# Kernel tuning notes

Hardware: AMD Instinct MI355X
Metric: run time of the kernel (lower is better)

## Reference

```python
import jax, jax.numpy as jnp
import numpy as np

B, S, HID = 2, 2048, 2048
NH, NKV, HD = 16, 8, 128
GROUPS = NH // NKV
EPS = 1e-6
SCALE = HD ** -0.5
ROPE_THETA = 1000000.0


def _rope_cos_sin(seq_len, head_dim, batch):
    inv_freq = 1.0 / (ROPE_THETA ** (np.arange(0, head_dim, 2, dtype=np.float32) / head_dim))
    t = np.arange(seq_len, dtype=np.float32)
    freqs = np.outer(t, inv_freq)                      # [S, HD/2]
    emb = np.concatenate([freqs, freqs], axis=-1)      # [S, HD]
    cos = np.broadcast_to(np.cos(emb), (batch, seq_len, head_dim))
    sin = np.broadcast_to(np.sin(emb), (batch, seq_len, head_dim))
    return jnp.asarray(cos), jnp.asarray(sin)


def setup_inputs() -> dict:
    key = jax.random.key(0)
    ks = jax.random.split(key, 6)
    hidden_states = jax.random.normal(ks[0], (B, S, HID), dtype=jnp.float32)
    cos, sin = _rope_cos_sin(S, HD, B)
    w_scale = HID ** -0.5
    Wq = jax.random.normal(ks[1], (NH * HD, HID), dtype=jnp.float32) * w_scale
    Wk = jax.random.normal(ks[2], (NKV * HD, HID), dtype=jnp.float32) * w_scale
    Wv = jax.random.normal(ks[3], (NKV * HD, HID), dtype=jnp.float32) * w_scale
    Wo = jax.random.normal(ks[4], (HID, NH * HD), dtype=jnp.float32) * w_scale
    q_norm_w = jnp.ones((HD,), dtype=jnp.float32)
    k_norm_w = jnp.ones((HD,), dtype=jnp.float32)
    return {"hidden_states": hidden_states, "cos": cos, "sin": sin,
            "Wq": Wq, "Wk": Wk, "Wv": Wv, "Wo": Wo,
            "q_norm_w": q_norm_w, "k_norm_w": k_norm_w}


def _rms_norm(x, w):
    # RMSNorm over last dim (head_dim), variance computed in fp32
    var = jnp.mean(x.astype(jnp.float32) ** 2, axis=-1, keepdims=True)
    return w * (x * jax.lax.rsqrt(var + EPS).astype(x.dtype))


def _rotate_half(x):
    x1, x2 = jnp.split(x, 2, axis=-1)
    return jnp.concatenate([-x2, x1], axis=-1)


def _apply_rope(x, cos, sin):
    # x: [B, H, S, D]; cos/sin: [B, S, D] -> unsqueeze head dim
    c = cos[:, None, :, :]
    s = sin[:, None, :, :]
    return x * c + _rotate_half(x) * s


def reference(hidden_states, cos, sin, Wq, Wk, Wv, Wo, q_norm_w, k_norm_w):
    b, s, _ = hidden_states.shape
    # QKV projections (bias=False per config.attention_bias)
    q = (hidden_states @ Wq.T).reshape(b, s, NH, HD)
    k = (hidden_states @ Wk.T).reshape(b, s, NKV, HD)
    v = (hidden_states @ Wv.T).reshape(b, s, NKV, HD)
    # Per-head QK RMSNorm, then [B, H, S, D]
    q = _rms_norm(q, q_norm_w).transpose(0, 2, 1, 3)
    k = _rms_norm(k, k_norm_w).transpose(0, 2, 1, 3)
    v = v.transpose(0, 2, 1, 3)
    # RoPE
    q = _apply_rope(q, cos, sin)
    k = _apply_rope(k, cos, sin)
    # GQA: expand kv heads to match query heads
    k = jnp.repeat(k, GROUPS, axis=1)
    v = jnp.repeat(v, GROUPS, axis=1)
    # SDPA (is_causal=False, mask=None, dropout=0)
    scores = jnp.einsum('bhqd,bhkd->bhqk', q, k) * SCALE
    probs = jax.nn.softmax(scores, axis=-1)
    attn = jnp.einsum('bhqk,bhkd->bhqd', probs, v)
    attn = attn.transpose(0, 2, 1, 3).reshape(b, s, NH * HD)
    return attn @ Wo.T
```

## Files before the change

kernel.cpp:

```cpp
#include <hip/hip_runtime.h>

using short8 = __attribute__((ext_vector_type(8))) short;
using f32x4  = __attribute__((ext_vector_type(4))) float;
using u32x2  = __attribute__((ext_vector_type(2))) unsigned int;
using u32x4  = __attribute__((ext_vector_type(4))) unsigned int;

#define MFMA16(a, b, c) __builtin_amdgcn_mfma_f32_16x16x32_bf16((a), (b), (c), 0, 0, 0)

__device__ inline float bf2f(ushort v) { return __uint_as_float(((unsigned int)v) << 16); }
__device__ inline unsigned int f2bfu(float f) {
  unsigned int u = __float_as_uint(f);
  return (u + 0x7fffu + ((u >> 16) & 1u)) >> 16;
}
__device__ inline unsigned int pk2(float a, float b) { return f2bfu(a) | (f2bfu(b) << 16); }

__device__ inline void gl_lds16(const ushort* g, ushort* l) {
  __builtin_amdgcn_global_load_lds(
      (const __attribute__((address_space(1))) void*)g,
      (__attribute__((address_space(3))) void*)l, 16, 0, 0);
}

__global__ __launch_bounds__(256) void f2b8(const float* __restrict__ src,
                                            ushort* __restrict__ dst, int n) {
  int i = (blockIdx.x * 256 + threadIdx.x) * 8;
  if (i >= n) return;
  f32x4 a = *(const f32x4*)(src + i);
  f32x4 b = *(const f32x4*)(src + i + 4);
  u32x4 o;
  o[0] = pk2(a[0], a[1]); o[1] = pk2(a[2], a[3]);
  o[2] = pk2(b[0], b[1]); o[3] = pk2(b[2], b[3]);
  *(u32x4*)(dst + i) = o;
}

#define GPHASE(CB, P, STG, VMW)                                                     \
  {                                                                                 \
    if (P == 0) {                                                                   \
      _Pragma("unroll") for (int n = 0; n < 4; ++n) {                               \
        bf[n][0] = *(const short8*)&L[(CB)*32768 + bBase + n*1024 + rdoff];         \
        bf[n][1] = *(const short8*)&L[(CB)*32768 + bBase + n*1024 + (rdoff ^ 32)];  \
      }                                                                             \
    }                                                                               \
    short8 af[2][2];                                                                \
    _Pragma("unroll") for (int mi = 0; mi < 2; ++mi) {                              \
      af[mi][0] = *(const short8*)&L[(CB)*32768 + aBase + ((P)*2+mi)*1024 + rdoff];        \
      af[mi][1] = *(const short8*)&L[(CB)*32768 + aBase + ((P)*2+mi)*1024 + (rdoff ^ 32)]; \
    }                                                                               \
    STG;                                                                            \
    __builtin_amdgcn_s_barrier();                                                   \
    asm volatile("s_waitcnt lgkmcnt(0)" ::: "memory");                              \
    __builtin_amdgcn_s_setprio(1);                                                  \
    _Pragma("unroll") for (int mi = 0; mi < 2; ++mi)                                \
      _Pragma("unroll") for (int n = 0; n < 4; ++n) {                               \
        acc[(P)*2+mi][n] = MFMA16(af[mi][0], bf[n][0], acc[(P)*2+mi][n]);           \
        acc[(P)*2+mi][n] = MFMA16(af[mi][1], bf[n][1], acc[(P)*2+mi][n]);           \
      }                                                                             \
    __builtin_amdgcn_s_setprio(0);                                                  \
    VMW;                                                                            \
    __builtin_amdgcn_s_barrier();                                                   \
  }

#define VM4 asm volatile("s_waitcnt vmcnt(4)" ::: "memory")
#define NOPX (void)0

template <int OUTF32>
__global__ __launch_bounds__(512, 2) void gemm256(const ushort* __restrict__ A,
                                                  const ushort* __restrict__ B,
                                                  void* __restrict__ Cv,
                                                  int M, int N, int K) {
  __shared__ ushort L[65536];
  const int t = threadIdx.x;
  const int w = t >> 6, l = t & 63, lr = l & 15, lg = l >> 4;
  const int wr = w >> 2, wc = w & 3;
  const int m0 = blockIdx.x * 256, n0 = blockIdx.y * 256;
  const int NT = K >> 6, NI = NT >> 1;

  f32x4 acc[8][4] = {};

  const int rdoff = lr * 64 + ((lg ^ (lr & 7)) * 8);
  const int aBase = wr * 8192;
  const int bBase = 16384 + (wc >> 1) * 8192 + (wc & 1) * 4096;

  const int ch0 = w * 2, ch1 = w * 2 + 1;
  const int srow0 = ch0 * 8 + (l >> 3), srow1 = ch1 * 8 + (l >> 3);
  const int scol = ((l & 7) ^ (l >> 3)) * 8;

  auto stage_a = [&](int h, int kt, int cb) {
    int ktc = kt < NT ? kt : NT - 1;
    gl_lds16(A + (size_t)(m0 + h * 128 + srow0) * K + ktc * 64 + scol,
             (ushort*)&L[cb * 32768 + h * 8192 + ch0 * 512]);
    gl_lds16(A + (size_t)(m0 + h * 128 + srow1) * K + ktc * 64 + scol,
             (ushort*)&L[cb * 32768 + h * 8192 + ch1 * 512]);
  };
  auto stage_b = [&](int h, int kt, int cb) {
    int ktc = kt < NT ? kt : NT - 1;
    gl_lds16(B + (size_t)(n0 + h * 128 + srow0) * K + ktc * 64 + scol,
             (ushort*)&L[cb * 32768 + 16384 + h * 8192 + ch0 * 512]);
    gl_lds16(B + (size_t)(n0 + h * 128 + srow1) * K + ktc * 64 + scol,
             (ushort*)&L[cb * 32768 + 16384 + h * 8192 + ch1 * 512]);
  };

  stage_a(0, 0, 0); stage_a(1, 0, 0); stage_b(0, 0, 0); stage_b(1, 0, 0);
  stage_b(0, 1, 1); stage_b(1, 1, 1);
  VM4;
  __builtin_amdgcn_s_barrier();

  short8 bf[4][2];
  for (int I = 0; I < NI; ++I) {
    const int t1 = 2 * I + 1, t2 = 2 * I + 2, t3 = 2 * I + 3;
    GPHASE(0, 0, stage_a(0, t1, 1), NOPX)
    GPHASE(0, 1, stage_a(1, t1, 1), NOPX)
    GPHASE(0, 2, stage_b(0, t2, 0), NOPX)
    GPHASE(0, 3, stage_b(1, t2, 0), VM4)
    GPHASE(1, 0, stage_a(0, t2, 0), NOPX)
    GPHASE(1, 1, stage_a(1, t2, 0), NOPX)
    GPHASE(1, 2, stage_b(0, t3, 1), NOPX)
    GPHASE(1, 3, stage_b(1, t3, 1), VM4)
  }

  const int crow0 = m0 + wr * 128 + lg * 4;
  const int ccol = n0 + wc * 64 + lr;
  if (OUTF32) {
    float* C = (float*)Cv;
#pragma unroll
    for (int m = 0; m < 8; ++m)
#pragma unroll
      for (int n = 0; n < 4; ++n)
#pragma unroll
        for (int j = 0; j < 4; ++j)
          C[(size_t)(crow0 + m * 16 + j) * N + ccol + n * 16] = acc[m][n][j];
  } else {
    ushort* C = (ushort*)Cv;
#pragma unroll
    for (int m = 0; m < 8; ++m)
#pragma unroll
      for (int n = 0; n < 4; ++n)
#pragma unroll
        for (int j = 0; j < 4; ++j)
          C[(size_t)(crow0 + m * 16 + j) * N + ccol + n * 16] = (ushort)f2bfu(acc[m][n][j]);
  }
}

__global__ __launch_bounds__(256) void qk_norm_rope(
    const ushort* __restrict__ QKVp, const float* __restrict__ cosb,
    const float* __restrict__ sinb, const float* __restrict__ qw,
    const float* __restrict__ kw, ushort* __restrict__ Qa, ushort* __restrict__ Ka) {
  int r = blockIdx.x * 4 + (threadIdx.x >> 6);
  int i = threadIdx.x & 63;
  int b, s, srccol;
  ushort* dst;
  const float* w;
  float scale;
  if (r < 65536) {
    b = r >> 15; int rem = r & 32767; s = rem >> 4; int h = rem & 15;
    srccol = h * 128;
    dst = Qa + ((size_t)((b * 16 + h) * 2048 + s)) * 128;
    w = qw;
    scale = 0.08838834764831845f * 1.4426950408889634f;
  } else {
    int rk = r - 65536;
    b = rk >> 14; int rem = rk & 16383; s = rem >> 3; int kvh = rem & 7;
    srccol = 2048 + kvh * 128;
    dst = Ka + ((size_t)((b * 8 + kvh) * 2048 + s)) * 128;
    w = kw;
    scale = 1.0f;
  }
  const ushort* src = QKVp + ((size_t)(b * 2048 + s)) * 4096 + srccol;
  float x0 = bf2f(src[i]), x1 = bf2f(src[i + 64]);
  float ss = x0 * x0 + x1 * x1;
#pragma unroll
  for (int m = 1; m < 64; m <<= 1) ss += __shfl_xor(ss, m);
  float inv = rsqrtf(ss * (1.0f / 128.0f) + 1e-6f);
  float xn0 = x0 * inv * w[i], xn1 = x1 * inv * w[i + 64];
  const float* cp = cosb + ((size_t)(b * 2048 + s)) * 128;
  const float* sp = sinb + ((size_t)(b * 2048 + s)) * 128;
  float o0 = (xn0 * cp[i] - xn1 * sp[i]) * scale;
  float o1 = (xn1 * cp[i + 64] + xn0 * sp[i + 64]) * scale;
  dst[i] = (ushort)f2bfu(o0);
  dst[i + 64] = (ushort)f2bfu(o1);
}

__global__ __launch_bounds__(256) void v_transpose(const ushort* __restrict__ QKVp,
                                                   ushort* __restrict__ Vt) {
  __shared__ ushort tile[64][136];
  int blk = blockIdx.x;
  int st = blk & 31, kvh = (blk >> 5) & 7, b = blk >> 8;
  int t = threadIdx.x;
  int s0 = st * 64;
  {
    int r = t >> 2, cseg = (t & 3) * 32;
    const ushort* src = QKVp + ((size_t)(b * 2048 + s0 + r)) * 4096 + 3072 + kvh * 128 + cseg;
#pragma unroll
    for (int i = 0; i < 4; ++i)
      *(uint4*)&tile[r][cseg + i * 8] = *(const uint4*)(src + i * 8);
  }
  __syncthreads();
  {
    int d = t >> 1, sh = (t & 1) * 32;
    ushort* dst = Vt + ((size_t)((b * 8 + kvh) * 128 + d)) * 2048 + s0 + sh;
    ushort buf[32];
#pragma unroll
    for (int k = 0; k < 32; ++k) buf[k] = tile[sh + k][d];
#pragma unroll
    for (int i = 0; i < 4; ++i) *(uint4*)(dst + i * 8) = *(uint4*)&buf[i * 8];
  }
}

__global__ __launch_bounds__(256, 2) void attn_kernel(const ushort* __restrict__ Qa,
                                                      const ushort* __restrict__ Ka,
                                                      const ushort* __restrict__ Vt,
                                                      ushort* __restrict__ Ctx) {
  __shared__ ushort Ks[64 * 128];
  __shared__ ushort Vs[128 * 64];
  __shared__ ushort Ps[8 * 1024];
  const int bh = blockIdx.x, b = bh >> 4, h = bh & 15, kvh = h >> 1;
  const int t = threadIdx.x, w = t >> 6, l = t & 63, lr = l & 15, lg = l >> 4;
  const int q0 = blockIdx.y * 128 + w * 32;
  const ushort* Qh = Qa + ((size_t)(b * 16 + h)) * 2048 * 128;
  const ushort* Kh = Ka + ((size_t)(b * 8 + kvh)) * 2048 * 128;
  const ushort* Vh = Vt + ((size_t)(b * 8 + kvh)) * 128 * 2048;

  short8 bq[2][4];
#pragma unroll
  for (int qt = 0; qt < 2; ++qt)
#pragma unroll
    for (int dc = 0; dc < 4; ++dc)
      bq[qt][dc] = *(const short8*)&Qh[(size_t)(q0 + qt * 16 + lr) * 128 + dc * 32 + lg * 8];

  f32x4 accO[8][2] = {};
  float mrun[2] = {-3.0e38f, -3.0e38f};
  float lrun[2] = {0.f, 0.f};

  for (int kt0 = 0; kt0 < 2048; kt0 += 64) {
    __syncthreads();
#pragma unroll
    for (int i = 0; i < 4; ++i) {
      const int c = w * 4 + i;
      const int krow = c * 4 + lg;
      gl_lds16(Kh + (size_t)(kt0 + krow) * 128 + (((l & 15) ^ (krow & 7)) * 8),
               &Ks[c * 512]);
      const int vrow = c * 8 + (l >> 3);
      gl_lds16(Vh + (size_t)vrow * 2048 + kt0 + (((l & 7) ^ ((l >> 3) & 7)) * 8),
               &Vs[c * 512]);
    }
    asm volatile("s_waitcnt vmcnt(0)" ::: "memory");
    __syncthreads();

    f32x4 accS[4][2] = {};
#pragma unroll
    for (int dc = 0; dc < 4; ++dc) {
      short8 ak[4];
#pragma unroll
      for (int kts = 0; kts < 4; ++kts)
        ak[kts] = *(const short8*)&Ks[(kts * 16 + lr) * 128 + ((dc * 4 + lg) ^ (lr & 7)) * 8];
#pragma unroll
      for (int kts = 0; kts < 4; ++kts)
#pragma unroll
        for (int qt = 0; qt < 2; ++qt)
          accS[kts][qt] = MFMA16(ak[kts], bq[qt][dc], accS[kts][qt]);
    }

#pragma unroll
    for (int qt = 0; qt < 2; ++qt) {
      float m0 = fmaxf(fmaxf(accS[0][qt][0], accS[0][qt][1]), fmaxf(accS[0][qt][2], accS[0][qt][3]));
      float m1 = fmaxf(fmaxf(accS[1][qt][0], accS[1][qt][1]), fmaxf(accS[1][qt][2], accS[1][qt][3]));
      float m2 = fmaxf(fmaxf(accS[2][qt][0], accS[2][qt][1]), fmaxf(accS[2][qt][2], accS[2][qt][3]));
      float m3 = fmaxf(fmaxf(accS[3][qt][0], accS[3][qt][1]), fmaxf(accS[3][qt][2], accS[3][qt][3]));
      float tm = fmaxf(fmaxf(m0, m1), fmaxf(m2, m3));
      tm = fmaxf(tm, __shfl_xor(tm, 16));
      tm = fmaxf(tm, __shfl_xor(tm, 32));
      if (!__all(tm <= mrun[qt] + 11.0f)) {
        float nm = fmaxf(mrun[qt], tm);
        float cf = exp2f(mrun[qt] - nm);
#pragma unroll
        for (int dc = 0; dc < 8; ++dc) {
          accO[dc][qt][0] *= cf; accO[dc][qt][1] *= cf;
          accO[dc][qt][2] *= cf; accO[dc][qt][3] *= cf;
        }
        lrun[qt] *= cf;
        mrun[qt] = nm;
      }
      float ts = 0.f;
#pragma unroll
      for (int kts = 0; kts < 4; ++kts)
#pragma unroll
        for (int j = 0; j < 4; ++j) {
          float p = exp2f(accS[kts][qt][j] - mrun[qt]);
          accS[kts][qt][j] = p;
          ts += p;
        }
      ts += __shfl_xor(ts, 16);
      ts += __shfl_xor(ts, 32);
      lrun[qt] += ts;
#pragma unroll
      for (int kts = 0; kts < 4; ++kts) {
        u32x2 pv;
        pv[0] = pk2(accS[kts][qt][0], accS[kts][qt][1]);
        pv[1] = pk2(accS[kts][qt][2], accS[kts][qt][3]);
        *(u32x2*)&Ps[(w * 2 + qt) * 1024 + lr * 64 +
                     (((kts * 2 + (lg >> 1)) ^ (lr & 7)) * 8 + (lg & 1) * 4)] = pv;
      }
    }
    asm volatile("s_waitcnt lgkmcnt(0)" ::: "memory");

    short8 bp[2][2];
#pragma unroll
    for (int qt = 0; qt < 2; ++qt)
#pragma unroll
      for (int ks = 0; ks < 2; ++ks)
        bp[qt][ks] = *(const short8*)&Ps[(w * 2 + qt) * 1024 + lr * 64 +
                                         ((ks * 4 + lg) ^ (lr & 7)) * 8];
#pragma unroll
    for (int dc = 0; dc < 8; ++dc) {
      short8 av[2];
#pragma unroll
      for (int ks = 0; ks < 2; ++ks)
        av[ks] = *(const short8*)&Vs[(dc * 16 + lr) * 64 + ((ks * 4 + lg) ^ (lr & 7)) * 8];
#pragma unroll
      for (int ks = 0; ks < 2; ++ks)
#pragma unroll
        for (int qt = 0; qt < 2; ++qt)
          accO[dc][qt] = MFMA16(av[ks], bp[qt][ks], accO[dc][qt]);
    }
  }

#pragma unroll
  for (int qt = 0; qt < 2; ++qt) {
    float inv = 1.0f / lrun[qt];
    int srow = q0 + qt * 16 + lr;
#pragma unroll
    for (int dc = 0; dc < 8; ++dc) {
      u32x2 ov;
      ov[0] = pk2(accO[dc][qt][0] * inv, accO[dc][qt][1] * inv);
      ov[1] = pk2(accO[dc][qt][2] * inv, accO[dc][qt][3] * inv);
      *(u32x2*)&Ctx[(size_t)(b * 2048 + srow) * 2048 + h * 128 + dc * 16 + lg * 4] = ov;
    }
  }
}

extern "C" void kernel_launch(void* const* d_in, const int* in_sizes, int n_in,
                              void* d_out, int out_size, void* d_ws, size_t ws_size,
                              hipStream_t stream) {
  const float* hidden = (const float*)d_in[0];
  const float* cosb   = (const float*)d_in[1];
  const float* sinb   = (const float*)d_in[2];
  const float* Wq     = (const float*)d_in[3];
  const float* Wk     = (const float*)d_in[4];
  const float* Wv     = (const float*)d_in[5];
  const float* Wo     = (const float*)d_in[6];
  const float* qw     = (const float*)d_in[7];
  const float* kw     = (const float*)d_in[8];

  char* ws = (char*)d_ws;
  ushort* Xb    = (ushort*)ws; ws += (size_t)4096 * 2048 * 2;
  ushort* Wcomb = (ushort*)ws; ws += (size_t)4096 * 2048 * 2;
  ushort* Wob   = (ushort*)ws; ws += (size_t)2048 * 2048 * 2;
  ushort* QKVp  = (ushort*)ws; ws += (size_t)4096 * 4096 * 2;
  ushort* Qa    = (ushort*)ws; ws += (size_t)2 * 16 * 2048 * 128 * 2;
  ushort* Ka    = (ushort*)ws; ws += (size_t)2 * 8 * 2048 * 128 * 2;
  ushort* Vt    = (ushort*)ws; ws += (size_t)2 * 8 * 2048 * 128 * 2;
  ushort* Ctx   = (ushort*)ws; ws += (size_t)4096 * 2048 * 2;

  f2b8<<<4096, 256, 0, stream>>>(hidden, Xb, 8388608);
  f2b8<<<2048, 256, 0, stream>>>(Wq, Wcomb, 4194304);
  f2b8<<<1024, 256, 0, stream>>>(Wk, Wcomb + 4194304, 2097152);
  f2b8<<<1024, 256, 0, stream>>>(Wv, Wcomb + 6291456, 2097152);
  f2b8<<<2048, 256, 0, stream>>>(Wo, Wob, 4194304);

  gemm256<0><<<dim3(16, 16), 512, 0, stream>>>(Xb, Wcomb, (void*)QKVp, 4096, 4096, 2048);

  qk_norm_rope<<<24576, 256, 0, stream>>>(QKVp, cosb, sinb, qw, kw, Qa, Ka);
  v_transpose<<<512, 256, 0, stream>>>(QKVp, Vt);

  attn_kernel<<<dim3(32, 16), 256, 0, stream>>>(Qa, Ka, Vt, Ctx);

  gemm256<1><<<dim3(16, 8), 512, 0, stream>>>(Ctx, Wob, d_out, 4096, 2048, 2048);
}
```

Baseline: 379.1 us.

## Double-buffer K/V tiles in attention kernel and use native exp2

```diff
diff --git a/kernel.cpp b/kernel.cpp
--- a/kernel.cpp
+++ b/kernel.cpp
@@ -209,8 +209,8 @@
                                                       const ushort* __restrict__ Ka,
                                                       const ushort* __restrict__ Vt,
                                                       ushort* __restrict__ Ctx) {
-  __shared__ ushort Ks[64 * 128];
-  __shared__ ushort Vs[128 * 64];
+  __shared__ ushort Ks[2][64 * 128];
+  __shared__ ushort Vs[2][128 * 64];
   __shared__ ushort Ps[8 * 1024];
   const int bh = blockIdx.x, b = bh >> 4, h = bh & 15, kvh = h >> 1;
   const int t = threadIdx.x, w = t >> 6, l = t & 63, lr = l & 15, lg = l >> 4;
@@ -225,33 +225,33 @@
 #pragma unroll
     for (int dc = 0; dc < 4; ++dc)
       bq[qt][dc] = *(const short8*)&Qh[(size_t)(q0 + qt * 16 + lr) * 128 + dc * 32 + lg * 8];
+  asm volatile("s_waitcnt vmcnt(0)" ::: "memory");
 
   f32x4 accO[8][2] = {};
   float mrun[2] = {-3.0e38f, -3.0e38f};
   float lrun[2] = {0.f, 0.f};
 
-  for (int kt0 = 0; kt0 < 2048; kt0 += 64) {
-    __syncthreads();
+  auto stage = [&](int kt0, ushort* KSB, ushort* VSB) {
 #pragma unroll
     for (int i = 0; i < 4; ++i) {
       const int c = w * 4 + i;
       const int krow = c * 4 + lg;
       gl_lds16(Kh + (size_t)(kt0 + krow) * 128 + (((l & 15) ^ (krow & 7)) * 8),
-               &Ks[c * 512]);
+               KSB + c * 512);
       const int vrow = c * 8 + (l >> 3);
       gl_lds16(Vh + (size_t)vrow * 2048 + kt0 + (((l & 7) ^ ((l >> 3) & 7)) * 8),
-               &Vs[c * 512]);
-    }
-    asm volatile("s_waitcnt vmcnt(0)" ::: "memory");
-    __syncthreads();
-
+               VSB + c * 512);
+    }
+  };
+
+  auto iter = [&](int kt, const ushort* KSB, const ushort* VSB, ushort* KSN, ushort* VSN) {
     f32x4 accS[4][2] = {};
 #pragma unroll
     for (int dc = 0; dc < 4; ++dc) {
       short8 ak[4];
 #pragma unroll
       for (int kts = 0; kts < 4; ++kts)
-        ak[kts] = *(const short8*)&Ks[(kts * 16 + lr) * 128 + ((dc * 4 + lg) ^ (lr & 7)) * 8];
+        ak[kts] = *(const short8*)&KSB[(kts * 16 + lr) * 128 + ((dc * 4 + lg) ^ (lr & 7)) * 8];
 #pragma unroll
       for (int kts = 0; kts < 4; ++kts)
 #pragma unroll
@@ -270,7 +270,7 @@
       tm = fmaxf(tm, __shfl_xor(tm, 32));
       if (!__all(tm <= mrun[qt] + 11.0f)) {
         float nm = fmaxf(mrun[qt], tm);
-        float cf = exp2f(mrun[qt] - nm);
+        float cf = __builtin_amdgcn_exp2f(mrun[qt] - nm);
 #pragma unroll
         for (int dc = 0; dc < 8; ++dc) {
           accO[dc][qt][0] *= cf; accO[dc][qt][1] *= cf;
@@ -284,7 +284,7 @@
       for (int kts = 0; kts < 4; ++kts)
 #pragma unroll
         for (int j = 0; j < 4; ++j) {
-          float p = exp2f(accS[kts][qt][j] - mrun[qt]);
+          float p = __builtin_amdgcn_exp2f(accS[kts][qt][j] - mrun[qt]);
           accS[kts][qt][j] = p;
           ts += p;
         }
@@ -314,13 +314,33 @@
       short8 av[2];
 #pragma unroll
       for (int ks = 0; ks < 2; ++ks)
-        av[ks] = *(const short8*)&Vs[(dc * 16 + lr) * 64 + ((ks * 4 + lg) ^ (lr & 7)) * 8];
+        av[ks] = *(const short8*)&VSB[(dc * 16 + lr) * 64 + ((ks * 4 + lg) ^ (lr & 7)) * 8];
 #pragma unroll
       for (int ks = 0; ks < 2; ++ks)
 #pragma unroll
         for (int qt = 0; qt < 2; ++qt)
           accO[dc][qt] = MFMA16(av[ks], bp[qt][ks], accO[dc][qt]);
     }
+
+    asm volatile("" ::: "memory");
+    __builtin_amdgcn_s_barrier();
+    if (kt + 128 <= 2048) {
+      stage(kt + 128, KSN, VSN);
+      asm volatile("s_waitcnt vmcnt(8)" ::: "memory");
+    } else {
+      asm volatile("s_waitcnt vmcnt(0)" ::: "memory");
+    }
+    __builtin_amdgcn_s_barrier();
+  };
+
+  stage(0, Ks[0], Vs[0]);
+  stage(64, Ks[1], Vs[1]);
+  asm volatile("s_waitcnt vmcnt(8)" ::: "memory");
+  __builtin_amdgcn_s_barrier();
+
+  for (int t2 = 0; t2 < 2048; t2 += 128) {
+    iter(t2,      Ks[0], Vs[0], Ks[0], Vs[0]);
+    iter(t2 + 64, Ks[1], Vs[1], Ks[1], Vs[1]);
   }
 
 #pragma unroll
```

After: 362.3 us. 4.4% less time.
